# Optimization experiments

Measured on AMD Instinct MI355X. Metric: run time of the kernel, lower is better.

Reference implementation:

```python
import jax, jax.numpy as jnp
import numpy as np

H, W, C = 384, 384, 200
HIDE, CNN_OUT, NCLS = 128, 64, 16
N = H * W
E = 1179648
EPS = 1e-5  # torch BatchNorm eps


def _bn(x, g, b, axes):
    # training-mode batch norm (biased variance), matches torch BN in train mode
    m = x.mean(axes, keepdims=True)
    v = x.var(axes, keepdims=True)
    return (x - m) * jax.lax.rsqrt(v + EPS) * g + b


def _gcn(x, w, bias, src, dst, n):
    # PyG GCNConv: add self loops, symmetric D^-1/2 (A+I) D^-1/2 normalization
    h = x @ w  # [N, out]
    loop = jnp.arange(n, dtype=src.dtype)
    s = jnp.concatenate([src, loop])
    d = jnp.concatenate([dst, loop])
    deg = jax.ops.segment_sum(jnp.ones(s.shape, x.dtype), d, num_segments=n)
    dinv = jnp.where(deg > 0, jax.lax.rsqrt(jnp.maximum(deg, 1.0)) * (deg > 0), 0.0)
    norm = dinv[s] * dinv[d]  # [E+N]
    out = jax.ops.segment_sum(h[s] * norm[:, None], d, num_segments=n)
    return out + bias


def _gnn_layer(x, bn_g, bn_b, w, b, src, dst):
    # F.normalize (row L2) -> BN1d -> GCNConv -> LeakyReLU (dropout off in eval)
    nrm = jnp.linalg.norm(x, axis=1, keepdims=True)
    x = x / jnp.maximum(nrm, 1e-12)
    x = _bn(x, bn_g, bn_b, (0,))
    return jax.nn.leaky_relu(_gcn(x, w, b, src, dst, x.shape[0]))


def setup_inputs() -> dict:
    key = jax.random.key(0)
    ks = jax.random.split(key, 16)
    p = {}
    p["x"] = jax.random.normal(ks[0], (H, W, C), jnp.float32)
    p["edge_index"] = jax.random.randint(ks[1], (2, E), 0, N, jnp.int32)
    # CNN_denoise: BN(C) -> 1x1 conv C->128 -> BN(128) -> 1x1 conv 128->128
    p["dn_bn1_g"] = jnp.ones((C,), jnp.float32); p["dn_bn1_b"] = jnp.zeros((C,), jnp.float32)
    p["dn_w1"] = jax.random.normal(ks[2], (C, HIDE), jnp.float32) * 0.05
    p["dn_b1"] = jnp.zeros((HIDE,), jnp.float32)
    p["dn_bn2_g"] = jnp.ones((HIDE,), jnp.float32); p["dn_bn2_b"] = jnp.zeros((HIDE,), jnp.float32)
    p["dn_w2"] = jax.random.normal(ks[3], (HIDE, HIDE), jnp.float32) * 0.05
    p["dn_b2"] = jnp.zeros((HIDE,), jnp.float32)
    # CNNCONV(128,64,k=5): BN(128) -> point 1x1 128->64 (no bias) -> depthwise 5x5 (bias)
    p["cnn_bn_g"] = jnp.ones((HIDE,), jnp.float32); p["cnn_bn_b"] = jnp.zeros((HIDE,), jnp.float32)
    p["cnn_pw"] = jax.random.normal(ks[4], (HIDE, CNN_OUT), jnp.float32) * 0.05
    p["cnn_dw"] = jax.random.normal(ks[5], (CNN_OUT, 1, 5, 5), jnp.float32) * 0.05
    p["cnn_db"] = jnp.zeros((CNN_OUT,), jnp.float32)
    # GCN branch: GNN(128,128), GNN(128,128), GNN(128,64)
    dims = [(HIDE, HIDE), (HIDE, HIDE), (HIDE, CNN_OUT)]
    for i, (di, do) in enumerate(dims, 1):
        p[f"g{i}_bn_g"] = jnp.ones((di,), jnp.float32)
        p[f"g{i}_bn_b"] = jnp.zeros((di,), jnp.float32)
        p[f"g{i}_w"] = jax.random.normal(ks[5 + i], (di, do), jnp.float32) * 0.05
        p[f"g{i}_b"] = jnp.zeros((do,), jnp.float32)
    p["lin_w"] = jax.random.normal(ks[9], (HIDE, NCLS), jnp.float32) * 0.05
    p["lin_b"] = jnp.zeros((NCLS,), jnp.float32)
    return p


def reference(x, edge_index,
              dn_bn1_g, dn_bn1_b, dn_w1, dn_b1, dn_bn2_g, dn_bn2_b, dn_w2, dn_b2,
              cnn_bn_g, cnn_bn_b, cnn_pw, cnn_dw, cnn_db,
              g1_bn_g, g1_bn_b, g1_w, g1_b,
              g2_bn_g, g2_bn_b, g2_w, g2_b,
              g3_bn_g, g3_bn_b, g3_w, g3_b,
              lin_w, lin_b):
    src, dst = edge_index[0], edge_index[1]
    # CNN_denoise (channel-last; 1x1 convs are matmuls)
    h = _bn(x, dn_bn1_g, dn_bn1_b, (0, 1))
    h = jax.nn.leaky_relu(h @ dn_w1 + dn_b1)
    h = _bn(h, dn_bn2_g, dn_bn2_b, (0, 1))
    clean = jax.nn.leaky_relu(h @ dn_w2 + dn_b2)       # [H,W,128]
    flat = clean.reshape(N, HIDE)
    # CNN branch: BN -> 1x1 -> LeakyReLU -> depthwise 5x5 -> LeakyReLU
    c = _bn(clean, cnn_bn_g, cnn_bn_b, (0, 1))
    c = jax.nn.leaky_relu(c @ cnn_pw)                  # [H,W,64]
    cn = c.transpose(2, 0, 1)[None]                    # [1,64,H,W]
    cn = jax.lax.conv_general_dilated(
        cn, cnn_dw, (1, 1), 'SAME', feature_group_count=CNN_OUT,
        dimension_numbers=('NCHW', 'OIHW', 'NCHW'))
    cn = jax.nn.leaky_relu(cn[0].transpose(1, 2, 0) + cnn_db)
    cnn_res = cn.reshape(N, CNN_OUT)
    # GCN branch (3 layers)
    g = _gnn_layer(flat, g1_bn_g, g1_bn_b, g1_w, g1_b, src, dst)
    g = _gnn_layer(g, g2_bn_g, g2_bn_b, g2_w, g2_b, src, dst)
    g = _gnn_layer(g, g3_bn_g, g3_bn_b, g3_w, g3_b, src, dst)
    y = jnp.concatenate([g, cnn_res], axis=-1) @ lin_w + lin_b
    return jax.nn.softmax(y, axis=-1)
```

## Files before the change

kernel.cpp:

```cpp
#include <hip/hip_runtime.h>
#include <stddef.h>

#define HH 384
#define WW 384
#define CC 200
#define NN 147456
#define EE 1179648
#define HIDE 128
#define COUT 64
#define NCLS 16
#define BN_EPS 1e-5f

using u16 = unsigned short;
typedef __attribute__((ext_vector_type(8))) short short8;
typedef __attribute__((ext_vector_type(4))) float float4v;

__device__ __forceinline__ float b2f(u16 u) {
    union { unsigned int i; float f; } v; v.i = ((unsigned int)u) << 16; return v.f;
}
__device__ __forceinline__ u16 f2b(float f) {
    union { float f; unsigned int i; } v; v.f = f;
    unsigned int x = v.i;
    unsigned int r = (x + 0x7fffu + ((x >> 16) & 1u)) >> 16;
    return (u16)r;
}
__device__ __forceinline__ float lrelu(float v) { return v > 0.f ? v : 0.01f * v; }

__global__ void sniff(const u16* __restrict__ x, int* __restrict__ flag) {
    __shared__ int cntS;
    if (threadIdx.x == 0) cntS = 0;
    __syncthreads();
    int c = 0;
    for (int i = 0; i < 8; i++) {
        u16 h = x[threadIdx.x * 8 + i];
        int hb = (h >> 8) & 0x7F;
        if (hb >= 0x3C && hb <= 0x41) c++;
    }
    atomicAdd(&cntS, c);
    __syncthreads();
    if (threadIdx.x == 0) *flag = (cntS < 1536) ? 1 : 0;
}

#define NPAR 27
struct PConv { const void* src[NPAR]; int n[NPAR]; int off[NPAR]; };

__global__ void convert_params(PConv pc, const int* __restrict__ flag,
                               u16* __restrict__ dst) {
    int b = blockIdx.x;
    int n = pc.n[b];
    const void* s = pc.src[b];
    u16* d = dst + pc.off[b];
    int isf = *flag;
    if (isf) {
        const float* sf = (const float*)s;
        for (int i = threadIdx.x; i < n; i += 256) d[i] = f2b(sf[i]);
    } else {
        const u16* sh = (const u16*)s;
        for (int i = threadIdx.x; i < n; i += 256) d[i] = sh[i];
    }
}

__global__ __launch_bounds__(256) void stats200(const void* __restrict__ X,
                                                const int* __restrict__ flag,
                                                float* __restrict__ arena) {
    __shared__ __align__(16) u16 s[128 * 200];
    int t = threadIdx.x;
    int r0 = blockIdx.x * 128;
    if (*flag) {
        const float* Xf = (const float*)X;
        for (int i = t; i < 128 * 25; i += 256) {
            int r = i / 25, kc = i - r * 25;
            const float* p = Xf + (size_t)(r0 + r) * CC + kc * 8;
            float4v a = *(const float4v*)p;
            float4v b = *(const float4v*)(p + 4);
            short8 v;
            #pragma unroll
            for (int j = 0; j < 4; j++) { v[j] = (short)f2b(a[j]); v[4 + j] = (short)f2b(b[j]); }
            *(short8*)&s[r * 200 + kc * 8] = v;
        }
    } else {
        const u16* Xh = (const u16*)X;
        for (int i = t; i < 128 * 25; i += 256) {
            int r = i / 25, kc = i - r * 25;
            *(short8*)&s[r * 200 + kc * 8] =
                *(const short8*)(Xh + (size_t)(r0 + r) * CC + kc * 8);
        }
    }
    __syncthreads();
    if (t < CC) {
        float sum = 0.f, sq = 0.f;
        for (int r = 0; r < 128; r++) {
            float v = b2f(s[r * 200 + t]);
            sum += v; sq += v * v;
        }
        atomicAdd(&arena[t], sum);
        atomicAdd(&arena[256 + t], sq);
    }
}

template<int K, int KPAD, int O>
__global__ __launch_bounds__(256) void fold_bn(
        const float* __restrict__ arena, float invN,
        const u16* __restrict__ bng, const u16* __restrict__ bnb,
        const u16* __restrict__ Wsrc, const u16* __restrict__ extrab,
        u16* __restrict__ WT, float* __restrict__ cb) {
    __shared__ float aS[KPAD], sS[KPAD];
    int t = threadIdx.x;
    if (t < KPAD) {
        float a = 0.f, sh = 0.f;
        if (t < K) {
            float m = arena[t] * invN;
            float var = fmaxf(arena[256 + t] * invN - m * m, 0.f);
            a = b2f(bng[t]) * rsqrtf(var + BN_EPS);
            sh = b2f(bnb[t]) - m * a;
        }
        aS[t] = a; sS[t] = sh;
    }
    __syncthreads();
    int g = t >> 6, l = t & 63;
    int o = blockIdx.x * 4 + g;
    if (o < O) {
        float c = 0.f;
        #pragma unroll
        for (int k = l; k < KPAD; k += 64) {
            float w = (k < K) ? b2f(Wsrc[k * O + o]) : 0.f;
            c += sS[k] * w;
            WT[o * KPAD + k] = f2b(aS[k] * w);
        }
        #pragma unroll
        for (int s = 32; s >= 1; s >>= 1) c += __shfl_down(c, s);
        if (l == 0) cb[o] = c + (extrab ? b2f(extrab[o]) : 0.f);
    }
}

template<int KT, int KSRC, int O, bool LEAKY, bool SCALE, int STATS>
__global__ __launch_bounds__(256) void gemm_mfma(
        const void* __restrict__ Ap, const u16* __restrict__ WT,
        const float* __restrict__ cb, const float* __restrict__ s1,
        const float* __restrict__ s2, const int* __restrict__ f32p,
        u16* __restrict__ out, float* __restrict__ stA,
        float* __restrict__ stB, float* __restrict__ invn) {
    constexpr int KPAD = KT * 32;
    constexpr int LDA = KPAD + 8;
    constexpr int CHR = KPAD / 8;
    constexpr int CHD = KSRC / 8;
    constexpr int NCT = O / 16;
    constexpr int CPW = NCT / 4;
    __shared__ __align__(16) u16 As[64 * LDA];
    __shared__ float rS[4][64];
    __shared__ float invS[64];
    __shared__ float sS1[64], sS2[64];
    int tid = threadIdx.x;
    int row0 = blockIdx.x * 64;

    int isf = f32p ? *f32p : 0;
    if (isf) {
        const float* A = (const float*)Ap;
        for (int i = tid; i < 64 * CHR; i += 256) {
            int r = i / CHR, kc = i - r * CHR;
            short8 v = {0, 0, 0, 0, 0, 0, 0, 0};
            if (kc < CHD) {
                const float* p = A + (size_t)(row0 + r) * KSRC + kc * 8;
                float4v a = *(const float4v*)p;
                float4v b = *(const float4v*)(p + 4);
                #pragma unroll
                for (int j = 0; j < 4; j++) { v[j] = (short)f2b(a[j]); v[4 + j] = (short)f2b(b[j]); }
            }
            *(short8*)&As[r * LDA + kc * 8] = v;
        }
    } else {
        const u16* A = (const u16*)Ap;
        for (int i = tid; i < 64 * CHR; i += 256) {
            int r = i / CHR, kc = i - r * CHR;
            short8 v = {0, 0, 0, 0, 0, 0, 0, 0};
            if (kc < CHD)
                v = *(const short8*)(A + (size_t)(row0 + r) * KSRC + kc * 8);
            *(short8*)&As[r * LDA + kc * 8] = v;
        }
    }
    if (SCALE && tid < 64) { sS1[tid] = s1[row0 + tid]; sS2[tid] = s2[row0 + tid]; }
    __syncthreads();

    int w = tid >> 6, lane = tid & 63, m = lane & 15, q = lane >> 4;
    float4v acc[4][CPW];
    #pragma unroll
    for (int mf = 0; mf < 4; mf++)
        #pragma unroll
        for (int cp = 0; cp < CPW; cp++)
            acc[mf][cp] = (float4v){0.f, 0.f, 0.f, 0.f};

    const u16* Abp = &As[m * LDA + q * 8];
    const u16* Bbp = WT + (size_t)((w * CPW) * 16 + m) * KPAD + q * 8;

    #pragma unroll
    for (int kt = 0; kt < KT; kt++) {
        short8 af[4];
        #pragma unroll
        for (int mf = 0; mf < 4; mf++)
            af[mf] = *(const short8*)(Abp + mf * 16 * LDA + kt * 32);
        #pragma unroll
        for (int cp = 0; cp < CPW; cp++) {
            short8 bf = *(const short8*)(Bbp + (size_t)cp * 16 * KPAD + kt * 32);
            #pragma unroll
            for (int mf = 0; mf < 4; mf++)
                acc[mf][cp] = __builtin_amdgcn_mfma_f32_16x16x32_bf16(
                    af[mf], bf, acc[mf][cp], 0, 0, 0);
        }
    }

    float rp[4][4] = {};
    #pragma unroll
    for (int cp = 0; cp < CPW; cp++) {
        int col = (w * CPW + cp) * 16 + m;
        float cbv = cb[col];
        #pragma unroll
        for (int mf = 0; mf < 4; mf++) {
            #pragma unroll
            for (int r = 0; r < 4; r++) {
                int rl = mf * 16 + q * 4 + r;
                float x = acc[mf][cp][r];
                if constexpr (SCALE) x = (x * sS1[rl] + cbv) * sS2[rl];
                else                 x += cbv;
                if constexpr (LEAKY) x = lrelu(x);
                out[(size_t)(row0 + rl) * O + col] = f2b(x);
                acc[mf][cp][r] = x;
                if constexpr (STATS == 2) rp[mf][r] += x * x;
            }
        }
    }

    if constexpr (STATS == 2) {
        #pragma unroll
        for (int mf = 0; mf < 4; mf++) {
            #pragma unroll
            for (int r = 0; r < 4; r++) {
                float v = rp[mf][r];
                v += __shfl_xor(v, 1); v += __shfl_xor(v, 2);
                v += __shfl_xor(v, 4); v += __shfl_xor(v, 8);
                if (m == 0) rS[w][mf * 16 + q * 4 + r] = v;
            }
        }
        __syncthreads();
        if (tid < 64) {
            float ss = rS[0][tid] + rS[1][tid] + rS[2][tid] + rS[3][tid];
            float inv = 1.0f / fmaxf(sqrtf(ss), 1e-12f);
            invS[tid] = inv;
            invn[row0 + tid] = inv;
        }
        __syncthreads();
    }

    if constexpr (STATS >= 1) {
        #pragma unroll
        for (int cp = 0; cp < CPW; cp++) {
            int col = (w * CPW + cp) * 16 + m;
            float cs = 0.f, cq = 0.f, ns = 0.f, nq = 0.f;
            #pragma unroll
            for (int mf = 0; mf < 4; mf++) {
                #pragma unroll
                for (int r = 0; r < 4; r++) {
                    float x = acc[mf][cp][r];
                    cs += x; cq += x * x;
                    if constexpr (STATS == 2) {
                        float nv = x * invS[mf * 16 + q * 4 + r];
                        ns += nv; nq += nv * nv;
                    }
                }
            }
            cs += __shfl_xor(cs, 16); cs += __shfl_xor(cs, 32);
            cq += __shfl_xor(cq, 16); cq += __shfl_xor(cq, 32);
            if constexpr (STATS == 2) {
                ns += __shfl_xor(ns, 16); ns += __shfl_xor(ns, 32);
                nq += __shfl_xor(nq, 16); nq += __shfl_xor(nq, 32);
            }
            if (q == 0) {
                atomicAdd(&stA[col], cs);
                atomicAdd(&stA[256 + col], cq);
                if constexpr (STATS == 2) {
                    atomicAdd(&stB[col], ns);
                    atomicAdd(&stB[256 + col], nq);
                }
            }
        }
    }
}

__global__ void hist(const int* __restrict__ dst, int* __restrict__ cnt) {
    int e = blockIdx.x * 256 + threadIdx.x;
    unsigned d = (unsigned)dst[e];
    if (d < (unsigned)NN) atomicAdd(&cnt[d], 1);
}
__global__ void mkdinv(const int* __restrict__ cnt, float* __restrict__ dinv) {
    int i = blockIdx.x * 256 + threadIdx.x;
    int c = cnt[i]; if (c < 0) c = 0;
    dinv[i] = rsqrtf((float)c + 1.0f);
}
__global__ void scan_part(const int* __restrict__ cnt, int* __restrict__ bsum) {
    int b = blockIdx.x, t = threadIdx.x;
    int base = b * 1024 + t * 4;
    int s = cnt[base] + cnt[base + 1] + cnt[base + 2] + cnt[base + 3];
    #pragma unroll
    for (int o = 32; o >= 1; o >>= 1) s += __shfl_down(s, o);
    __shared__ int ws4[4];
    if ((t & 63) == 0) ws4[t >> 6] = s;
    __syncthreads();
    if (t == 0) bsum[b] = ws4[0] + ws4[1] + ws4[2] + ws4[3];
}
__global__ void scan_top(const int* __restrict__ bsum, int* __restrict__ boff) {
    if (threadIdx.x == 0) {
        int a = 0;
        for (int i = 0; i < 144; i++) { boff[i] = a; a += bsum[i]; }
    }
}
__global__ void scan_write(const int* __restrict__ cnt, const int* __restrict__ boff,
                           int* __restrict__ offv) {
    int b = blockIdx.x, t = threadIdx.x;
    int base = b * 1024 + t * 4;
    int v0 = cnt[base], v1 = cnt[base + 1], v2 = cnt[base + 2], v3 = cnt[base + 3];
    int ts = v0 + v1 + v2 + v3;
    __shared__ int sc[256];
    sc[t] = ts;
    __syncthreads();
    for (int o = 1; o < 256; o <<= 1) {
        int x = (t >= o) ? sc[t - o] : 0;
        __syncthreads();
        sc[t] += x;
        __syncthreads();
    }
    int excl = boff[b] + sc[t] - ts;
    offv[base] = excl;
    offv[base + 1] = excl + v0;
    offv[base + 2] = excl + v0 + v1;
    offv[base + 3] = excl + v0 + v1 + v2;
    if (b == 143 && t == 255) offv[NN] = excl + ts;
}
__global__ void scatter(const int* __restrict__ src, const int* __restrict__ dst,
                        int* __restrict__ cursor, const int* __restrict__ offv,
                        int* __restrict__ csr) {
    int e = blockIdx.x * 256 + threadIdx.x;
    unsigned d = (unsigned)dst[e];
    if (d >= (unsigned)NN) return;
    int p = atomicAdd(&cursor[d], 1);
    unsigned idx = (unsigned)(offv[d] + p);
    if (idx < (unsigned)EE) csr[idx] = src[e];
}

template<int O, int STATS, int GRP>
__global__ __launch_bounds__(256) void aggregate(
        const u16* __restrict__ h2, const int* __restrict__ offv,
        const int* __restrict__ csr, const float* __restrict__ dinv,
        const u16* __restrict__ gb, u16* __restrict__ outp,
        float* __restrict__ stA, float* __restrict__ invn) {
    constexpr int CH = O / 8;
    constexpr int NPB = 256 / CH;
    __shared__ float colS[O], colQ[O];
    int t = threadIdx.x;
    if (STATS && t < O) { colS[t] = 0.f; colQ[t] = 0.f; }
    int local = t / CH, c = t % CH;
    size_t cof = (size_t)c * 8;
    short8 gv = *(const short8*)(gb + cof);
    float sreg[8] = {0.f, 0.f, 0.f, 0.f, 0.f, 0.f, 0.f, 0.f};
    float qreg[8] = {0.f, 0.f, 0.f, 0.f, 0.f, 0.f, 0.f, 0.f};

    #pragma unroll
    for (int g = 0; g < GRP; g++) {
        int d = blockIdx.x * (NPB * GRP) + g * NPB + local;
        float acc[8];
        short8 selfv = *(const short8*)(h2 + (size_t)d * O + cof);
        #pragma unroll
        for (int j = 0; j < 8; j++) acc[j] = b2f((u16)selfv[j]);
        int e0 = offv[d], e1 = offv[d + 1];
        if (e0 < 0) e0 = 0;
        if (e1 > EE) e1 = EE;
        int k = e0;
        for (; k + 2 <= e1; k += 2) {
            unsigned sa = (unsigned)csr[k];
            unsigned sb = (unsigned)csr[k + 1];
            short8 va = {0, 0, 0, 0, 0, 0, 0, 0};
            short8 vb = {0, 0, 0, 0, 0, 0, 0, 0};
            if (sa < (unsigned)NN) va = *(const short8*)(h2 + (size_t)sa * O + cof);
            if (sb < (unsigned)NN) vb = *(const short8*)(h2 + (size_t)sb * O + cof);
            #pragma unroll
            for (int j = 0; j < 8; j++) acc[j] += b2f((u16)va[j]) + b2f((u16)vb[j]);
        }
        if (k < e1) {
            unsigned sa = (unsigned)csr[k];
            if (sa < (unsigned)NN) {
                short8 va = *(const short8*)(h2 + (size_t)sa * O + cof);
                #pragma unroll
                for (int j = 0; j < 8; j++) acc[j] += b2f((u16)va[j]);
            }
        }
        float dd = dinv[d];
        float outv[8];
        short8 res;
        #pragma unroll
        for (int j = 0; j < 8; j++) {
            outv[j] = lrelu(dd * acc[j] + b2f((u16)gv[j]));
            res[j] = (short)f2b(outv[j]);
        }
        *(short8*)(outp + (size_t)d * O + cof) = res;

        if constexpr (STATS) {
            float ss = 0.f;
            #pragma unroll
            for (int j = 0; j < 8; j++) ss += outv[j] * outv[j];
            ss += __shfl_xor(ss, 1); ss += __shfl_xor(ss, 2);
            ss += __shfl_xor(ss, 4); ss += __shfl_xor(ss, 8);
            float inv = 1.0f / fmaxf(sqrtf(ss), 1e-12f);
            if (c == 0) invn[d] = inv;
            #pragma unroll
            for (int j = 0; j < 8; j++) {
                float nv = outv[j] * inv;
                sreg[j] += nv; qreg[j] += nv * nv;
            }
        }
    }

    if constexpr (STATS) {
        __syncthreads();
        #pragma unroll
        for (int j = 0; j < 8; j++) {
            float s = sreg[j];
            s += __shfl_xor(s, 16); s += __shfl_xor(s, 32);
            float qq = qreg[j];
            qq += __shfl_xor(qq, 16); qq += __shfl_xor(qq, 32);
            if ((t & 63) < 16) {
                atomicAdd(&colS[c * 8 + j], s);
                atomicAdd(&colQ[c * 8 + j], qq);
            }
        }
        __syncthreads();
        if (t < O) {
            atomicAdd(&stA[t], colS[t]);
            atomicAdd(&stA[256 + t], colQ[t]);
        }
    }
}

__global__ __launch_bounds__(256) void final_fused(
        const u16* __restrict__ g3, const u16* __restrict__ cpre,
        const u16* __restrict__ dwW, const u16* __restrict__ db,
        const u16* __restrict__ lw, const u16* __restrict__ lb,
        const int* __restrict__ flag, void* __restrict__ outp) {
    __shared__ __align__(16) u16 tile[400 * 72];
    __shared__ __align__(16) u16 wT[25 * 64];
    __shared__ __align__(16) u16 wL[2048];
    __shared__ float bDW[64];
    __shared__ float bL[16];
    int t = threadIdx.x;
    int tx = blockIdx.x % 24, ty = blockIdx.x / 24;
    int x0 = tx * 16 - 2, y0 = ty * 16 - 2;
    for (int i = t; i < 1600; i += 256) {
        int f = i / 25, tap = i - f * 25;
        wT[tap * 64 + f] = dwW[i];
    }
    for (int i = t; i < 2048; i += 256) wL[i] = lw[i];
    if (t < 64) bDW[t] = b2f(db[t]);
    if (t < 16) bL[t] = b2f(lb[t]);
    for (int u = t; u < 3200; u += 256) {
        int pix = u >> 3, c8 = u & 7;
        int gy = y0 + pix / 20, gx = x0 + pix % 20;
        short8 v = {0, 0, 0, 0, 0, 0, 0, 0};
        if (gy >= 0 && gy < HH && gx >= 0 && gx < WW)
            v = *(const short8*)(cpre + ((size_t)(gy * WW + gx)) * 64 + c8 * 8);
        *(short8*)&tile[pix * 72 + c8 * 8] = v;
    }
    __syncthreads();

    int px = t & 15, py = t >> 4;
    int node = (ty * 16 + py) * WW + tx * 16 + px;
    float y[16];
    #pragma unroll
    for (int o = 0; o < 16; o++) y[o] = bL[o];

    const u16* g3p = g3 + (size_t)node * 64;
    for (int c8 = 0; c8 < 8; c8++) {
        short8 gvv = *(const short8*)(g3p + c8 * 8);
        #pragma unroll
        for (int j = 0; j < 8; j++) {
            float g = b2f((u16)gvv[j]);
            const short8 w0 = *(const short8*)&wL[(c8 * 8 + j) * 16];
            const short8 w1 = *(const short8*)&wL[(c8 * 8 + j) * 16 + 8];
            #pragma unroll
            for (int o = 0; o < 8; o++) {
                y[o]     += g * b2f((u16)w0[o]);
                y[o + 8] += g * b2f((u16)w1[o]);
            }
        }
    }
    for (int c8 = 0; c8 < 8; c8++) {
        float acc[8] = {0.f, 0.f, 0.f, 0.f, 0.f, 0.f, 0.f, 0.f};
        #pragma unroll
        for (int dy = 0; dy < 5; dy++) {
            int rbase = ((py + dy) * 20 + px) * 72 + c8 * 8;
            #pragma unroll
            for (int dx = 0; dx < 5; dx++) {
                short8 v  = *(const short8*)&tile[rbase + dx * 72];
                short8 wv = *(const short8*)&wT[(dy * 5 + dx) * 64 + c8 * 8];
                #pragma unroll
                for (int j = 0; j < 8; j++)
                    acc[j] += b2f((u16)v[j]) * b2f((u16)wv[j]);
            }
        }
        #pragma unroll
        for (int j = 0; j < 8; j++) {
            float cv = lrelu(acc[j] + bDW[c8 * 8 + j]);
            int f = 64 + c8 * 8 + j;
            const short8 w0 = *(const short8*)&wL[f * 16];
            const short8 w1 = *(const short8*)&wL[f * 16 + 8];
            #pragma unroll
            for (int o = 0; o < 8; o++) {
                y[o]     += cv * b2f((u16)w0[o]);
                y[o + 8] += cv * b2f((u16)w1[o]);
            }
        }
    }
    float mx = y[0];
    #pragma unroll
    for (int o = 1; o < 16; o++) mx = fmaxf(mx, y[o]);
    float sum = 0.f;
    #pragma unroll
    for (int o = 0; o < 16; o++) { y[o] = __expf(y[o] - mx); sum += y[o]; }
    float inv = 1.0f / fmaxf(sum, 1e-30f);
    if (*flag) {
        float* of = (float*)outp;
        #pragma unroll
        for (int o = 0; o < 16; o++) of[(size_t)node * 16 + o] = y[o] * inv;
    } else {
        u16* oh = (u16*)outp;
        #pragma unroll
        for (int o = 0; o < 16; o++) oh[(size_t)node * 16 + o] = f2b(y[o] * inv);
    }
}

extern "C" void kernel_launch(void* const* d_in, const int* in_sizes, int n_in,
                              void* d_out, int out_size, void* d_ws, size_t ws_size,
                              hipStream_t stream) {
    const void* X   = d_in[0];
    const int* EIDX = (const int*)d_in[1];
    const int* esrc = EIDX;
    const int* edst = EIDX + EE;

    char* ws = (char*)d_ws;
    size_t off = 0;
    auto alloc = [&](size_t sz) -> char* {
        size_t szr = (sz + 255) & ~(size_t)255;
        char* p;
        if (off + szr <= ws_size) { p = ws + off; off += szr; }
        else { p = ws; }
        return p;
    };

    int*   dflag   = (int*)alloc(256);
    static const int pidx[NPAR] = {2,3,4,5,6,7,8,9,10,11,12,13,14,
                                   15,16,17,18,19,20,21,22,23,24,25,26,27,28};
    static const int pn[NPAR]   = {200,200,25600,128,128,128,16384,128,
                                   128,128,8192,1600,64,
                                   128,128,16384,128,
                                   128,128,16384,128,
                                   128,128,8192,64,
                                   2048,16};
    u16* parena = (u16*)alloc(100352 * 2);
    PConv pc;
    {
        int po = 0;
        for (int i = 0; i < NPAR; i++) {
            pc.src[i] = d_in[pidx[i]];
            pc.n[i] = pn[i];
            pc.off[i] = po;
            po += (pn[i] + 15) & ~15;
        }
    }
    const u16* DN1G = parena + pc.off[0];
    const u16* DN1B = parena + pc.off[1];
    const u16* DNW1 = parena + pc.off[2];
    const u16* DNB1 = parena + pc.off[3];
    const u16* DN2G = parena + pc.off[4];
    const u16* DN2B = parena + pc.off[5];
    const u16* DNW2 = parena + pc.off[6];
    const u16* DNB2 = parena + pc.off[7];
    const u16* CBNG = parena + pc.off[8];
    const u16* CBNB = parena + pc.off[9];
    const u16* CPW  = parena + pc.off[10];
    const u16* CDW  = parena + pc.off[11];
    const u16* CDB  = parena + pc.off[12];
    const u16* G1G  = parena + pc.off[13];
    const u16* G1B  = parena + pc.off[14];
    const u16* G1W  = parena + pc.off[15];
    const u16* G1BI = parena + pc.off[16];
    const u16* G2G  = parena + pc.off[17];
    const u16* G2B  = parena + pc.off[18];
    const u16* G2W  = parena + pc.off[19];
    const u16* G2BI = parena + pc.off[20];
    const u16* G3G  = parena + pc.off[21];
    const u16* G3B  = parena + pc.off[22];
    const u16* G3W  = parena + pc.off[23];
    const u16* G3BI = parena + pc.off[24];
    const u16* LINW = parena + pc.off[25];
    const u16* LINB = parena + pc.off[26];

    int*   cnt     = (int*)alloc((size_t)NN * 4);
    int*   cursor  = (int*)alloc((size_t)NN * 4);
    float* arena   = (float*)alloc(6 * 512 * 4);
    int*   offv    = (int*)alloc((size_t)(NN + 1) * 4);
    int*   bsum    = (int*)alloc(144 * 4);
    int*   boff    = (int*)alloc(144 * 4);
    float* dinvp   = (float*)alloc((size_t)NN * 4);
    float* invnorm = (float*)alloc((size_t)NN * 4);
    u16*   W1T     = (u16*)alloc(128 * 224 * 2);
    u16*   W2T     = (u16*)alloc(128 * 128 * 2);
    u16*   WpwT    = (u16*)alloc(64 * 128 * 2);
    u16*   WgT     = (u16*)alloc(128 * 128 * 2);
    float* cb1     = (float*)alloc(128 * 4);
    float* cb2     = (float*)alloc(128 * 4);
    float* cb3     = (float*)alloc(128 * 4);
    float* cbg     = (float*)alloc(128 * 4);
    int*   csr     = (int*)alloc((size_t)EE * 4);
    u16*   cbuf    = (u16*)alloc((size_t)NN * 64 * 2);
    u16*   big1    = (u16*)alloc((size_t)NN * 128 * 2);
    u16*   big2    = (u16*)alloc((size_t)NN * 128 * 2);

    const float invN = 1.0f / (float)NN;
    size_t zsz = (size_t)((char*)(arena + 6 * 512) - (char*)cnt);
    size_t zcap = ((char*)cnt >= ws && (size_t)((char*)cnt - ws) < ws_size)
                      ? ws_size - (size_t)((char*)cnt - ws) : 0;
    if (zsz > zcap) zsz = zcap;
    hipMemsetAsync(cnt, 0, zsz, stream);

    sniff<<<1, 256, 0, stream>>>((const u16*)X, dflag);
    convert_params<<<NPAR, 256, 0, stream>>>(pc, dflag, parena);

    hist<<<EE / 256, 256, 0, stream>>>(edst, cnt);
    mkdinv<<<NN / 256, 256, 0, stream>>>(cnt, dinvp);
    scan_part<<<144, 256, 0, stream>>>(cnt, bsum);
    scan_top<<<1, 64, 0, stream>>>(bsum, boff);
    scan_write<<<144, 256, 0, stream>>>(cnt, boff, offv);
    scatter<<<EE / 256, 256, 0, stream>>>(esrc, edst, cursor, offv, csr);

    stats200<<<1152, 256, 0, stream>>>(X, dflag, arena + 0 * 512);
    fold_bn<200, 224, 128><<<32, 256, 0, stream>>>(arena + 0 * 512, invN, DN1G, DN1B, DNW1, DNB1, W1T, cb1);
    gemm_mfma<7, 200, 128, true, false, 1><<<NN / 64, 256, 0, stream>>>(
        X, W1T, cb1, nullptr, nullptr, dflag, big1, arena + 1 * 512, nullptr, nullptr);
    fold_bn<128, 128, 128><<<32, 256, 0, stream>>>(arena + 1 * 512, invN, DN2G, DN2B, DNW2, DNB2, W2T, cb2);
    gemm_mfma<4, 128, 128, true, false, 2><<<NN / 64, 256, 0, stream>>>(
        big1, W2T, cb2, nullptr, nullptr, nullptr, big2, arena + 2 * 512, arena + 3 * 512, invnorm);

    fold_bn<128, 128, 64><<<16, 256, 0, stream>>>(arena + 2 * 512, invN, CBNG, CBNB, CPW, nullptr, WpwT, cb3);
    gemm_mfma<4, 128, 64, true, false, 0><<<NN / 64, 256, 0, stream>>>(
        big2, WpwT, cb3, nullptr, nullptr, nullptr, cbuf, nullptr, nullptr, nullptr);

    fold_bn<128, 128, 128><<<32, 256, 0, stream>>>(arena + 3 * 512, invN, G1G, G1B, G1W, nullptr, WgT, cbg);
    gemm_mfma<4, 128, 128, false, true, 0><<<NN / 64, 256, 0, stream>>>(
        big2, WgT, cbg, invnorm, dinvp, nullptr, big1, nullptr, nullptr, nullptr);
    aggregate<128, 1, 4><<<NN / 64, 256, 0, stream>>>(
        big1, offv, csr, dinvp, G1BI, big2, arena + 4 * 512, invnorm);

    fold_bn<128, 128, 128><<<32, 256, 0, stream>>>(arena + 4 * 512, invN, G2G, G2B, G2W, nullptr, WgT, cbg);
    gemm_mfma<4, 128, 128, false, true, 0><<<NN / 64, 256, 0, stream>>>(
        big2, WgT, cbg, invnorm, dinvp, nullptr, big1, nullptr, nullptr, nullptr);
    aggregate<128, 1, 4><<<NN / 64, 256, 0, stream>>>(
        big1, offv, csr, dinvp, G2BI, big2, arena + 5 * 512, invnorm);

    fold_bn<128, 128, 64><<<16, 256, 0, stream>>>(arena + 5 * 512, invN, G3G, G3B, G3W, nullptr, WgT, cbg);
    gemm_mfma<4, 128, 64, false, true, 0><<<NN / 64, 256, 0, stream>>>(
        big2, WgT, cbg, invnorm, dinvp, nullptr, big1, nullptr, nullptr, nullptr);
    aggregate<64, 0, 1><<<NN / 32, 256, 0, stream>>>(
        big1, offv, csr, dinvp, G3BI, big2, nullptr, nullptr);

    final_fused<<<576, 256, 0, stream>>>(big2, cbuf, CDW, CDB, LINW, LINB, dflag, d_out);

    (void)in_sizes; (void)n_in; (void)out_size;
}
```

Baseline: 925.4 us.

## Fuse CNN pointwise GEMM into first GCN GEMM and unroll aggregate gather by four

Merges the CNN branch's 1x1 pointwise GEMM (128->64) with the first GCN layer's weight GEMM (128->128) into one 192-column GEMM. Columns are split in the epilogue, each half with its own scale or LeakyReLU and its own output buffer. This reads big2 once instead of twice and removes one kernel launch. Separately, the aggregate gather loop now issues four neighbour loads per iteration and drops the per-edge bounds checks, which raises memory-level parallelism but trusts that every csr index is valid. The wider GEMM tile (12 column tiles across 4 waves) raises accumulator register pressure.

Result: no change. 922.3 us (-0.3%).

```diff
diff --git a/kernel.cpp b/kernel.cpp
--- a/kernel.cpp
+++ b/kernel.cpp
@@ -133,13 +133,14 @@
     }
 }
 
-template<int KT, int KSRC, int O, bool LEAKY, bool SCALE, int STATS>
+template<int KT, int KSRC, int O, bool LEAKY, bool SCALE, int STATS, bool DUAL>
 __global__ __launch_bounds__(256) void gemm_mfma(
         const void* __restrict__ Ap, const u16* __restrict__ WT,
         const float* __restrict__ cb, const float* __restrict__ s1,
         const float* __restrict__ s2, const int* __restrict__ f32p,
         u16* __restrict__ out, float* __restrict__ stA,
-        float* __restrict__ stB, float* __restrict__ invn) {
+        float* __restrict__ stB, float* __restrict__ invn,
+        u16* __restrict__ out2) {
     constexpr int KPAD = KT * 32;
     constexpr int LDA = KPAD + 8;
     constexpr int CHR = KPAD / 8;
@@ -211,7 +212,8 @@
     float rp[4][4] = {};
     #pragma unroll
     for (int cp = 0; cp < CPW; cp++) {
-        int col = (w * CPW + cp) * 16 + m;
+        int ct = w * CPW + cp;
+        int col = ct * 16 + m;
         float cbv = cb[col];
         #pragma unroll
         for (int mf = 0; mf < 4; mf++) {
@@ -219,10 +221,20 @@
             for (int r = 0; r < 4; r++) {
                 int rl = mf * 16 + q * 4 + r;
                 float x = acc[mf][cp][r];
-                if constexpr (SCALE) x = (x * sS1[rl] + cbv) * sS2[rl];
-                else                 x += cbv;
-                if constexpr (LEAKY) x = lrelu(x);
-                out[(size_t)(row0 + rl) * O + col] = f2b(x);
+                if constexpr (DUAL) {
+                    if (ct < 8) {
+                        x = (x * sS1[rl] + cbv) * sS2[rl];
+                        out[(size_t)(row0 + rl) * 128 + col] = f2b(x);
+                    } else {
+                        x = lrelu(x + cbv);
+                        out2[(size_t)(row0 + rl) * 64 + (col - 128)] = f2b(x);
+                    }
+                } else {
+                    if constexpr (SCALE) x = (x * sS1[rl] + cbv) * sS2[rl];
+                    else                 x += cbv;
+                    if constexpr (LEAKY) x = lrelu(x);
+                    out[(size_t)(row0 + rl) * O + col] = f2b(x);
+                }
                 acc[mf][cp][r] = x;
                 if constexpr (STATS == 2) rp[mf][r] += x * x;
             }
@@ -358,6 +370,7 @@
     if (STATS && t < O) { colS[t] = 0.f; colQ[t] = 0.f; }
     int local = t / CH, c = t % CH;
     size_t cof = (size_t)c * 8;
+    const u16* hb = h2 + cof;
     short8 gv = *(const short8*)(gb + cof);
     float sreg[8] = {0.f, 0.f, 0.f, 0.f, 0.f, 0.f, 0.f, 0.f};
     float qreg[8] = {0.f, 0.f, 0.f, 0.f, 0.f, 0.f, 0.f, 0.f};
@@ -366,30 +379,42 @@
     for (int g = 0; g < GRP; g++) {
         int d = blockIdx.x * (NPB * GRP) + g * NPB + local;
         float acc[8];
-        short8 selfv = *(const short8*)(h2 + (size_t)d * O + cof);
+        short8 selfv = *(const short8*)(hb + (size_t)d * O);
         #pragma unroll
         for (int j = 0; j < 8; j++) acc[j] = b2f((u16)selfv[j]);
         int e0 = offv[d], e1 = offv[d + 1];
         if (e0 < 0) e0 = 0;
         if (e1 > EE) e1 = EE;
         int k = e0;
-        for (; k + 2 <= e1; k += 2) {
+        for (; k + 4 <= e1; k += 4) {
             unsigned sa = (unsigned)csr[k];
             unsigned sb = (unsigned)csr[k + 1];
-            short8 va = {0, 0, 0, 0, 0, 0, 0, 0};
-            short8 vb = {0, 0, 0, 0, 0, 0, 0, 0};
-            if (sa < (unsigned)NN) va = *(const short8*)(h2 + (size_t)sa * O + cof);
-            if (sb < (unsigned)NN) vb = *(const short8*)(h2 + (size_t)sb * O + cof);
-            #pragma unroll
-            for (int j = 0; j < 8; j++) acc[j] += b2f((u16)va[j]) + b2f((u16)vb[j]);
+            unsigned sc2 = (unsigned)csr[k + 2];
+            unsigned sd = (unsigned)csr[k + 3];
+            short8 va = *(const short8*)(hb + (size_t)sa * O);
+            short8 vb = *(const short8*)(hb + (size_t)sb * O);
+            short8 vc = *(const short8*)(hb + (size_t)sc2 * O);
+            short8 vd = *(const short8*)(hb + (size_t)sd * O);
+            #pragma unroll
+            for (int j = 0; j < 8; j++)
+                acc[j] += (b2f((u16)va[j]) + b2f((u16)vb[j])) +
+                          (b2f((u16)vc[j]) + b2f((u16)vd[j]));
+        }
+        if (k + 2 <= e1) {
+            unsigned sa = (unsigned)csr[k];
+            unsigned sb = (unsigned)csr[k + 1];
+            short8 va = *(const short8*)(hb + (size_t)sa * O);
+            short8 vb = *(const short8*)(hb + (size_t)sb * O);
+            #pragma unroll
+            for (int j = 0; j < 8; j++)
+                acc[j] += b2f((u16)va[j]) + b2f((u16)vb[j]);
+            k += 2;
         }
         if (k < e1) {
             unsigned sa = (unsigned)csr[k];
-            if (sa < (unsigned)NN) {
-                short8 va = *(const short8*)(h2 + (size_t)sa * O + cof);
-                #pragma unroll
-                for (int j = 0; j < 8; j++) acc[j] += b2f((u16)va[j]);
-            }
+            short8 va = *(const short8*)(hb + (size_t)sa * O);
+            #pragma unroll
+            for (int j = 0; j < 8; j++) acc[j] += b2f((u16)va[j]);
         }
         float dd = dinv[d];
         float outv[8];
@@ -610,12 +635,10 @@
     float* invnorm = (float*)alloc((size_t)NN * 4);
     u16*   W1T     = (u16*)alloc(128 * 224 * 2);
     u16*   W2T     = (u16*)alloc(128 * 128 * 2);
-    u16*   WpwT    = (u16*)alloc(64 * 128 * 2);
-    u16*   WgT     = (u16*)alloc(128 * 128 * 2);
+    u16*   WgT     = (u16*)alloc(192 * 128 * 2);
     float* cb1     = (float*)alloc(128 * 4);
     float* cb2     = (float*)alloc(128 * 4);
-    float* cb3     = (float*)alloc(128 * 4);
-    float* cbg     = (float*)alloc(128 * 4);
+    float* cbg     = (float*)alloc(192 * 4);
     int*   csr     = (int*)alloc((size_t)EE * 4);
     u16*   cbuf    = (u16*)alloc((size_t)NN * 64 * 2);
     u16*   big1    = (u16*)alloc((size_t)NN * 128 * 2);
@@ -640,31 +663,29 @@
 
     stats200<<<1152, 256, 0, stream>>>(X, dflag, arena + 0 * 512);
     fold_bn<200, 224, 128><<<32, 256, 0, stream>>>(arena + 0 * 512, invN, DN1G, DN1B, DNW1, DNB1, W1T, cb1);
-    gemm_mfma<7, 200, 128, true, false, 1><<<NN / 64, 256, 0, stream>>>(
-        X, W1T, cb1, nullptr, nullptr, dflag, big1, arena + 1 * 512, nullptr, nullptr);
+    gemm_mfma<7, 200, 128, true, false, 1, false><<<NN / 64, 256, 0, stream>>>(
+        X, W1T, cb1, nullptr, nullptr, dflag, big1, arena + 1 * 512, nullptr, nullptr, nullptr);
     fold_bn<128, 128, 128><<<32, 256, 0, stream>>>(arena + 1 * 512, invN, DN2G, DN2B, DNW2, DNB2, W2T, cb2);
-    gemm_mfma<4, 128, 128, true, false, 2><<<NN / 64, 256, 0, stream>>>(
-        big1, W2T, cb2, nullptr, nullptr, nullptr, big2, arena + 2 * 512, arena + 3 * 512, invnorm);
-
-    fold_bn<128, 128, 64><<<16, 256, 0, stream>>>(arena + 2 * 512, invN, CBNG, CBNB, CPW, nullptr, WpwT, cb3);
-    gemm_mfma<4, 128, 64, true, false, 0><<<NN / 64, 256, 0, stream>>>(
-        big2, WpwT, cb3, nullptr, nullptr, nullptr, cbuf, nullptr, nullptr, nullptr);
+    gemm_mfma<4, 128, 128, true, false, 2, false><<<NN / 64, 256, 0, stream>>>(
+        big1, W2T, cb2, nullptr, nullptr, nullptr, big2, arena + 2 * 512, arena + 3 * 512, invnorm, nullptr);
 
     fold_bn<128, 128, 128><<<32, 256, 0, stream>>>(arena + 3 * 512, invN, G1G, G1B, G1W, nullptr, WgT, cbg);
-    gemm_mfma<4, 128, 128, false, true, 0><<<NN / 64, 256, 0, stream>>>(
-        big2, WgT, cbg, invnorm, dinvp, nullptr, big1, nullptr, nullptr, nullptr);
+    fold_bn<128, 128, 64><<<16, 256, 0, stream>>>(arena + 2 * 512, invN, CBNG, CBNB, CPW, nullptr,
+                                                  WgT + 128 * 128, cbg + 128);
+    gemm_mfma<4, 128, 192, false, true, 0, true><<<NN / 64, 256, 0, stream>>>(
+        big2, WgT, cbg, invnorm, dinvp, nullptr, big1, nullptr, nullptr, nullptr, cbuf);
     aggregate<128, 1, 4><<<NN / 64, 256, 0, stream>>>(
         big1, offv, csr, dinvp, G1BI, big2, arena + 4 * 512, invnorm);
 
     fold_bn<128, 128, 128><<<32, 256, 0, stream>>>(arena + 4 * 512, invN, G2G, G2B, G2W, nullptr, WgT, cbg);
-    gemm_mfma<4, 128, 128, false, true, 0><<<NN / 64, 256, 0, stream>>>(
-        big2, WgT, cbg, invnorm, dinvp, nullptr, big1, nullptr, nullptr, nullptr);
+    gemm_mfma<4, 128, 128, false, true, 0, false><<<NN / 64, 256, 0, stream>>>(
+        big2, WgT, cbg, invnorm, dinvp, nullptr, big1, nullptr, nullptr, nullptr, nullptr);
     aggregate<128, 1, 4><<<NN / 64, 256, 0, stream>>>(
         big1, offv, csr, dinvp, G2BI, big2, arena + 5 * 512, invnorm);
 
     fold_bn<128, 128, 64><<<16, 256, 0, stream>>>(arena + 5 * 512, invN, G3G, G3B, G3W, nullptr, WgT, cbg);
-    gemm_mfma<4, 128, 64, false, true, 0><<<NN / 64, 256, 0, stream>>>(
-        big2, WgT, cbg, invnorm, dinvp, nullptr, big1, nullptr, nullptr, nullptr);
+    gemm_mfma<4, 128, 64, false, true, 0, false><<<NN / 64, 256, 0, stream>>>(
+        big2, WgT, cbg, invnorm, dinvp, nullptr, big1, nullptr, nullptr, nullptr, nullptr);
     aggregate<64, 0, 1><<<NN / 32, 256, 0, stream>>>(
         big1, offv, csr, dinvp, G3BI, big2, nullptr, nullptr);
 
```
